# Performance work log

Measured on AMD Instinct MI355X. Metric: run time of the kernel, lower is better.

## Reference

```python
import jax, jax.numpy as jnp
import numpy as np

B = 512
AUDIO_H, VIDEO_H, TEXT_H = 64, 64, 128
POST_DIM = 128
FUSION_DIM = (TEXT_H + 1) * (VIDEO_H + 1) * (AUDIO_H + 1)  # 129*65*65 = 545025


def setup_inputs() -> dict:
    key = jax.random.key(0)
    ks = jax.random.split(key, 9)
    s1 = 1.0 / np.sqrt(FUSION_DIM)
    s2 = 1.0 / np.sqrt(POST_DIM)
    return {
        "audio_h": jax.random.normal(ks[0], (B, AUDIO_H), jnp.float32),
        "video_h": jax.random.normal(ks[1], (B, VIDEO_H), jnp.float32),
        "text_h": jax.random.normal(ks[2], (B, TEXT_H), jnp.float32),
        "W1": jax.random.uniform(ks[3], (FUSION_DIM, POST_DIM), jnp.float32, -s1, s1),
        "b1": jax.random.uniform(ks[4], (POST_DIM,), jnp.float32, -s1, s1),
        "W2": jax.random.uniform(ks[5], (POST_DIM, POST_DIM), jnp.float32, -s2, s2),
        "b2": jax.random.uniform(ks[6], (POST_DIM,), jnp.float32, -s2, s2),
        "W3": jax.random.uniform(ks[7], (POST_DIM, 1), jnp.float32, -s2, s2),
        "b3": jax.random.uniform(ks[8], (1,), jnp.float32, -s2, s2),
    }


def reference(audio_h, video_h, text_h, W1, b1, W2, b2, W3, b3):
    b = audio_h.shape[0]
    ones = jnp.ones((b, 1), audio_h.dtype)
    a1 = jnp.concatenate([ones, audio_h], axis=1)  # [B, A+1]
    v1 = jnp.concatenate([ones, video_h], axis=1)  # [B, V+1]
    t1 = jnp.concatenate([ones, text_h], axis=1)   # [B, T+1]
    # trilinear outer product: [B, T+1, V+1, A+1]
    fusion = jnp.einsum('bi,bj,bk->bijk', t1, v1, a1)
    flat = fusion.reshape(b, -1)  # [B, FUSION_DIM]
    # post-fusion MLP (dropout probs = 0 -> identity at inference)
    y1 = jax.nn.relu(flat @ W1 + b1)
    y2 = jax.nn.relu(y1 @ W2 + b2)
    y3 = jax.nn.sigmoid(y2 @ W3 + b3)
    # affine map to [-3, 3]: output_range=6, output_shift=-3
    return y3 * 6.0 - 3.0
```

## Files before the change

kernel.cpp:

```cpp
#include <hip/hip_runtime.h>
#include <hip/hip_bf16.h>
#include <math.h>

#define POST 128
#define NI 129
#define NJK 4225
#define NTOT 16512
#define KBLKS 134
#define MBLKS 32
#define KSTEPS32 133
#define PANEL_CLAMP 2163184u

typedef __attribute__((ext_vector_type(8))) short bf16x8;
typedef __attribute__((ext_vector_type(4))) float f32x4;
typedef __attribute__((ext_vector_type(4))) unsigned int u32x4;

__device__ __forceinline__ unsigned short f2bf(float f){
    unsigned u = __builtin_bit_cast(unsigned, f);
    unsigned r = (u + 0x7FFFu + ((u >> 16) & 1u)) >> 16;
    return (unsigned short)r;
}
__device__ __forceinline__ unsigned pack2(float a, float b){
    return (unsigned)f2bf(a) | ((unsigned)f2bf(b) << 16);
}
__device__ __forceinline__ unsigned cvtpk(float lo, float hi){
    unsigned r;
    asm("v_cvt_pk_bf16_f32 %0, %1, %2" : "=v"(r) : "v"(lo), "v"(hi));
    return r;
}

__device__ __forceinline__ void gload16(const void* g, void* l){
    __builtin_amdgcn_global_load_lds(
        (const __attribute__((address_space(1))) unsigned int*)g,
        (__attribute__((address_space(3))) unsigned int*)l, 16, 0, 0);
}

__global__ void build_af(const float* __restrict__ audio,
                         const float* __restrict__ video,
                         uint4* __restrict__ af)
{
    int gid = blockIdx.x * 256 + threadIdx.x;
    if (gid >= KBLKS * MBLKS * 64) return;
    int lane = gid & 63;
    int mblk = (gid >> 6) & 31;
    int kblk = gid >> 11;
    int m  = mblk * 16 + (lane & 15);
    int k0 = kblk * 32 + (lane >> 4) * 8;
    float vals[8];
#pragma unroll
    for (int j = 0; j < 8; ++j){
        int k = k0 + j;
        float p = 0.f;
        if (k < NJK){
            int jj = k / 65;
            int kk = k - jj * 65;
            float a = (kk == 0) ? 1.f : audio[m * 64 + kk - 1];
            float v = (jj == 0) ? 1.f : video[m * 64 + jj - 1];
            p = a * v;
        }
        vals[j] = p;
    }
    uint4 o;
    o.x = pack2(vals[0], vals[1]);
    o.y = pack2(vals[2], vals[3]);
    o.z = pack2(vals[4], vals[5]);
    o.w = pack2(vals[6], vals[7]);
    af[gid] = o;
}

__global__ __launch_bounds__(256, 3) void fusion_gemm(
    const float* __restrict__ W1,
    const uint4* __restrict__ af,
    float* __restrict__ Z)
{
    __shared__ __align__(16) char lds[49152];

    int orig = blockIdx.x;
    int xcd  = orig & 7;
    int base = (xcd < 4) ? xcd * 65 : 260 + (xcd - 4) * 64;
    int w    = base + (orig >> 3);
    int nt = w >> 2;
    int mt = w & 3;

    int t    = threadIdx.x;
    int lane = t & 63;
    int wv   = t >> 6;
    int wm   = wv >> 1, wn = wv & 1;

    f32x4 acc[4][4] = {};

    const char* wpanel = (const char*)(W1 + (size_t)nt * (NJK * 128));
    const char* afb    = (const char*)af;

#define STAGE(ks_, pb_)                                                         \
    do {                                                                        \
        char* dstA_ = lds + (pb_) * 8192;                                       \
        char* dstB_ = lds + 16384 + (pb_) * 16384;                              \
        _Pragma("unroll")                                                       \
        for (int i_ = 0; i_ < 6; ++i_){                                         \
            int c_ = wv * 6 + i_;                                               \
            if (c_ < 8){                                                        \
                const char* s_ = afb + (size_t)(ks_) * 32768                    \
                               + (size_t)(mt * 8 + c_) * 1024 + lane * 16;      \
                gload16(s_, dstA_ + c_ * 1024);                                 \
            } else {                                                            \
                int cb_ = c_ - 8;                                               \
                int k_  = 2 * cb_ + (lane >> 5);                                \
                int ngs_ = (lane & 31) ^ (((k_ >> 3) & 1) << 2);                \
                unsigned bo_ = (unsigned)(ks_) * 16384u                         \
                             + (unsigned)k_ * 512u + (unsigned)ngs_ * 16u;      \
                if (bo_ > PANEL_CLAMP) bo_ = PANEL_CLAMP;        \
                gload16(wpanel + bo_, dstB_ + cb_ * 1024);                      \
            }                                                                   \
        }                                                                       \
    } while (0)

    STAGE(0, 0);

    for (int ks = 0; ks < KSTEPS32; ++ks){
        int p = ks & 1;

        if (ks + 1 < KSTEPS32){
            STAGE(ks + 1, p ^ 1);
            asm volatile("s_waitcnt vmcnt(6)" ::: "memory");
        } else {
            asm volatile("s_waitcnt vmcnt(0)" ::: "memory");
        }
        __builtin_amdgcn_s_barrier();

        {
            const char* sa   = lds + p * 8192;
            const char* rawp = lds + 16384 + p * 16384;

            bf16x8 a[4], b[4];
#pragma unroll
            for (int f = 0; f < 4; ++f)
                a[f] = *(const bf16x8*)(sa + (wm * 4 + f) * 1024 + lane * 16);

            int h  = lane >> 4;
            int fx = (h & 1) << 2;
#pragma unroll
            for (int g = 0; g < 4; ++g){
                int n = wn * 64 + g * 16 + (lane & 15);
                const char* bp = rawp + (h * 8) * 512
                               + (((n >> 2) ^ fx) * 16) + (n & 3) * 4;
                float v[8];
#pragma unroll
                for (int j = 0; j < 8; ++j)
                    v[j] = *(const float*)(bp + j * 512);
                u32x4 ub;
                ub.x = cvtpk(v[0], v[1]);
                ub.y = cvtpk(v[2], v[3]);
                ub.z = cvtpk(v[4], v[5]);
                ub.w = cvtpk(v[6], v[7]);
                b[g] = __builtin_bit_cast(bf16x8, ub);
            }

#pragma unroll
            for (int f = 0; f < 4; ++f)
#pragma unroll
                for (int g = 0; g < 4; ++g)
                    acc[f][g] = __builtin_amdgcn_mfma_f32_16x16x32_bf16(a[f], b[g], acc[f][g], 0, 0, 0);
        }

        __builtin_amdgcn_sched_barrier(0);
        __builtin_amdgcn_s_barrier();
    }

    int row0 = mt * 128 + wm * 64 + (lane >> 4) * 4;
    int col0 = nt * 128 + wn * 64 + (lane & 15);
#pragma unroll
    for (int f = 0; f < 4; ++f)
#pragma unroll
        for (int g = 0; g < 4; ++g)
#pragma unroll
            for (int r = 0; r < 4; ++r)
                Z[(size_t)(row0 + f * 16 + r) * NTOT + col0 + g * 16] = acc[f][g][r];
}

__global__ void tail_mlp(const float* __restrict__ Z,
                         const float* __restrict__ text,
                         const float* __restrict__ b1,
                         const float* __restrict__ W2,
                         const float* __restrict__ b2,
                         const float* __restrict__ W3,
                         const float* __restrict__ b3,
                         float* __restrict__ out)
{
    int b   = blockIdx.x;
    int tid = threadIdx.x;
    __shared__ float t1s[NI];
    __shared__ float y1s[POST];
    __shared__ float red[2];

    t1s[tid + 1] = text[b * 128 + tid];
    if (tid == 0) t1s[0] = 1.f;
    __syncthreads();

    const float* zrow = Z + (size_t)b * NTOT;
    float acc = 0.f;
    for (int i = 0; i < NI; ++i)
        acc = fmaf(t1s[i], zrow[i * 128 + tid], acc);
    acc += b1[tid];
    float y1 = fmaxf(acc, 0.f);
    y1s[tid] = y1;
    __syncthreads();

    float a2 = b2[tid];
    for (int q = 0; q < 128; ++q)
        a2 = fmaf(y1s[q], W2[q * 128 + tid], a2);
    float y2 = fmaxf(a2, 0.f);

    float part = y2 * W3[tid];
#pragma unroll
    for (int off = 32; off > 0; off >>= 1)
        part += __shfl_down(part, off);
    if ((tid & 63) == 0) red[tid >> 6] = part;
    __syncthreads();
    if (tid == 0){
        float z = red[0] + red[1] + b3[0];
        out[b] = 6.f / (1.f + expf(-z)) - 3.f;
    }
}

extern "C" void kernel_launch(void* const* d_in, const int* in_sizes, int n_in,
                              void* d_out, int out_size, void* d_ws, size_t ws_size,
                              hipStream_t stream)
{
    const float* audio = (const float*)d_in[0];
    const float* video = (const float*)d_in[1];
    const float* text  = (const float*)d_in[2];
    const float* W1    = (const float*)d_in[3];
    const float* b1    = (const float*)d_in[4];
    const float* W2    = (const float*)d_in[5];
    const float* b2    = (const float*)d_in[6];
    const float* W3    = (const float*)d_in[7];
    const float* b3    = (const float*)d_in[8];
    float* out = (float*)d_out;

    char* ws = (char*)d_ws;
    uint4* af = (uint4*)ws;
    float* Z  = (float*)(ws + (8u << 20));

    int af_granules = KBLKS * MBLKS * 64;
    build_af<<<(af_granules + 255) / 256, 256, 0, stream>>>(audio, video, af);
    fusion_gemm<<<516, 256, 0, stream>>>(W1, af, Z);
    tail_mlp<<<512, 128, 0, stream>>>(Z, text, b1, W2, b2, W3, b3, out);
}
```

Before: 156.0 us.

## Load A fragments directly to registers and triple-buffer W1 panel in LDS

The A operand (audio×video bf16 fragments) is now loaded straight from global memory into registers, one k-step ahead, instead of being staged through LDS. The freed LDS space is used to triple-buffer the W1 panel, prefetching two k-steps ahead with adjusted vmcnt waits. This is meant to deepen the pipeline on the dominant W1 stream and cut LDS traffic for A. In exchange it uses more registers and adds global loads of A per wave, since both wn waves now fetch the same A rows.

```diff
diff --git a/kernel.cpp b/kernel.cpp
--- a/kernel.cpp
+++ b/kernel.cpp
@@ -90,55 +90,61 @@
     f32x4 acc[4][4] = {};
 
     const char* wpanel = (const char*)(W1 + (size_t)nt * (NJK * 128));
-    const char* afb    = (const char*)af;
 
 #define STAGE(ks_, pb_)                                                         \
     do {                                                                        \
-        char* dstA_ = lds + (pb_) * 8192;                                       \
-        char* dstB_ = lds + 16384 + (pb_) * 16384;                              \
+        char* dstB_ = lds + (pb_) * 16384;                                      \
         _Pragma("unroll")                                                       \
-        for (int i_ = 0; i_ < 6; ++i_){                                         \
-            int c_ = wv * 6 + i_;                                               \
-            if (c_ < 8){                                                        \
-                const char* s_ = afb + (size_t)(ks_) * 32768                    \
-                               + (size_t)(mt * 8 + c_) * 1024 + lane * 16;      \
-                gload16(s_, dstA_ + c_ * 1024);                                 \
-            } else {                                                            \
-                int cb_ = c_ - 8;                                               \
-                int k_  = 2 * cb_ + (lane >> 5);                                \
-                int ngs_ = (lane & 31) ^ (((k_ >> 3) & 1) << 2);                \
-                unsigned bo_ = (unsigned)(ks_) * 16384u                         \
-                             + (unsigned)k_ * 512u + (unsigned)ngs_ * 16u;      \
-                if (bo_ > PANEL_CLAMP) bo_ = PANEL_CLAMP;        \
-                gload16(wpanel + bo_, dstB_ + cb_ * 1024);                      \
-            }                                                                   \
+        for (int i_ = 0; i_ < 4; ++i_){                                         \
+            int cb_ = wv * 4 + i_;                                              \
+            int k_  = 2 * cb_ + (lane >> 5);                                    \
+            int ngs_ = (lane & 31) ^ (((k_ >> 3) & 1) << 2);                    \
+            unsigned bo_ = (unsigned)(ks_) * 16384u                             \
+                         + (unsigned)k_ * 512u + (unsigned)ngs_ * 16u;          \
+            if (bo_ > PANEL_CLAMP) bo_ = PANEL_CLAMP;            \
+            gload16(wpanel + bo_, dstB_ + cb_ * 1024);                          \
         }                                                                       \
     } while (0)
 
+#define ALOAD(ks_, d0, d1, d2, d3)                                             \
+    do {                                                                        \
+        const uint4* ab_ = af + ((size_t)(ks_) * 32 + mt * 8 + wm * 4) * 64 + lane; \
+        d0 = ab_[0]; d1 = ab_[64]; d2 = ab_[128]; d3 = ab_[192];                \
+    } while (0)
+
+    uint4 aC0, aC1, aC2, aC3, aN0, aN1, aN2, aN3;
+
     STAGE(0, 0);
+    STAGE(1, 1);
+    ALOAD(0, aC0, aC1, aC2, aC3);
+
+    int p = 0, q = 2;
 
     for (int ks = 0; ks < KSTEPS32; ++ks){
-        int p = ks & 1;
-
-        if (ks + 1 < KSTEPS32){
-            STAGE(ks + 1, p ^ 1);
-            asm volatile("s_waitcnt vmcnt(6)" ::: "memory");
+        if (ks + 1 < KSTEPS32)
+            ALOAD(ks + 1, aN0, aN1, aN2, aN3);
+        __builtin_amdgcn_sched_barrier(0);
+
+        if (ks + 2 < KSTEPS32)
+            STAGE(ks + 2, q);
+        __builtin_amdgcn_sched_barrier(0);
+
+        if (ks + 2 < KSTEPS32){
+            asm volatile("s_waitcnt vmcnt(16)" ::: "memory");
+        } else if (ks + 1 < KSTEPS32){
+            asm volatile("s_waitcnt vmcnt(12)" ::: "memory");
         } else {
-            asm volatile("s_waitcnt vmcnt(0)" ::: "memory");
+            asm volatile("s_waitcnt vmcnt(4)" ::: "memory");
         }
+        __builtin_amdgcn_sched_barrier(0);
         __builtin_amdgcn_s_barrier();
 
         {
-            const char* sa   = lds + p * 8192;
-            const char* rawp = lds + 16384 + p * 16384;
-
-            bf16x8 a[4], b[4];
-#pragma unroll
-            for (int f = 0; f < 4; ++f)
-                a[f] = *(const bf16x8*)(sa + (wm * 4 + f) * 1024 + lane * 16);
-
+            const char* rawp = lds + p * 16384;
             int h  = lane >> 4;
             int fx = (h & 1) << 2;
+
+            bf16x8 b[4];
 #pragma unroll
             for (int g = 0; g < 4; ++g){
                 int n = wn * 64 + g * 16 + (lane & 15);
@@ -156,15 +162,25 @@
                 b[g] = __builtin_bit_cast(bf16x8, ub);
             }
 
-#pragma unroll
-            for (int f = 0; f < 4; ++f)
-#pragma unroll
-                for (int g = 0; g < 4; ++g)
-                    acc[f][g] = __builtin_amdgcn_mfma_f32_16x16x32_bf16(a[f], b[g], acc[f][g], 0, 0, 0);
+            bf16x8 a0 = __builtin_bit_cast(bf16x8, aC0);
+            bf16x8 a1 = __builtin_bit_cast(bf16x8, aC1);
+            bf16x8 a2 = __builtin_bit_cast(bf16x8, aC2);
+            bf16x8 a3 = __builtin_bit_cast(bf16x8, aC3);
+#pragma unroll
+            for (int g = 0; g < 4; ++g){
+                acc[0][g] = __builtin_amdgcn_mfma_f32_16x16x32_bf16(a0, b[g], acc[0][g], 0, 0, 0);
+                acc[1][g] = __builtin_amdgcn_mfma_f32_16x16x32_bf16(a1, b[g], acc[1][g], 0, 0, 0);
+                acc[2][g] = __builtin_amdgcn_mfma_f32_16x16x32_bf16(a2, b[g], acc[2][g], 0, 0, 0);
+                acc[3][g] = __builtin_amdgcn_mfma_f32_16x16x32_bf16(a3, b[g], acc[3][g], 0, 0, 0);
+            }
         }
 
         __builtin_amdgcn_sched_barrier(0);
         __builtin_amdgcn_s_barrier();
+
+        aC0 = aN0; aC1 = aN1; aC2 = aN2; aC3 = aN3;
+        p = (p == 2) ? 0 : p + 1;
+        q = (q == 2) ? 0 : q + 1;
     }
 
     int row0 = mt * 128 + wm * 64 + (lane >> 4) * 4;
```

Measured after the change: 181.1 us. 1.16x slower.
